# Kernel tuning notes

Hardware: AMD Instinct MI355X
Metric: run time of the kernel (lower is better)

The kernel has to match this reference:

```python
import jax, jax.numpy as jnp
import numpy as np

D_MODEL = 1024
HEAD = 16
K_D = D_MODEL // HEAD
SEQ_LEN = 2048
BATCH = 4
NEG = 1e10


def setup_inputs() -> dict:
    key = jax.random.key(0)
    ks = jax.random.split(key, 5)
    x = jax.random.normal(ks[0], (BATCH, SEQ_LEN, D_MODEL), dtype=jnp.float32)
    # params (torch Linear stored as [out,in]; we store [in,out] and matmul directly)
    W_attn = jax.random.normal(ks[1], (D_MODEL, 3 * D_MODEL), dtype=jnp.float32) * 0.02
    b_attn = jnp.zeros((3 * D_MODEL,), dtype=jnp.float32)
    W_proj = jax.random.normal(ks[2], (D_MODEL, D_MODEL), dtype=jnp.float32) * 0.02
    b_proj = jnp.zeros((D_MODEL,), dtype=jnp.float32)
    return {"x": x, "W_attn": W_attn, "b_attn": b_attn, "W_proj": W_proj, "b_proj": b_proj}


def reference(x, W_attn, b_attn, W_proj, b_proj):
    B, S, D = x.shape
    qkv = x @ W_attn + b_attn                     # [B,S,3D]
    # NOTE: source splits as (value, query, key) in that order
    value, query, key = jnp.split(qkv, 3, axis=-1)

    def heads(t):  # [B,S,D] -> [B,H,S,k_d]
        return t.reshape(B, S, HEAD, K_D).transpose(0, 2, 1, 3)

    v, q, k = heads(value), heads(query), heads(key)
    present = jnp.stack((k, v))                   # [2,B,H,S,k_d]

    scores = jnp.einsum('bhqd,bhkd->bhqk', q, k) / jnp.sqrt(jnp.float32(K_D))
    bias = jnp.tril(jnp.ones((S, S), dtype=scores.dtype))[None, None]
    scores = scores * bias - NEG * (1.0 - bias)
    attn = jax.nn.softmax(scores, axis=-1)
    out = jnp.einsum('bhqk,bhkd->bhqd', attn, v)  # [B,H,S,k_d]
    out = out.transpose(0, 2, 1, 3).reshape(B, S, D)
    out = out @ W_proj + b_proj
    return out, present
```

## Files before the change

kernel.cpp:

```cpp
#include <hip/hip_runtime.h>

typedef __attribute__((ext_vector_type(8))) short short8;
typedef __attribute__((ext_vector_type(4))) short short4v;
typedef __attribute__((ext_vector_type(4))) float f32x4;
typedef __attribute__((ext_vector_type(16))) float f32x16;
typedef __attribute__((ext_vector_type(4))) unsigned int u32x4;
typedef __attribute__((ext_vector_type(2))) unsigned int u32x2;
typedef unsigned int u32;

#define D_MODEL 1024
#define HEADS 16
#define KD 64
#define SEQ 2048
#define BATCH 4
#define NTOK (BATCH*SEQ)
#define QKV_N (3*D_MODEL)

__device__ inline float bf2f(unsigned short u) {
    unsigned x = ((unsigned)u) << 16;
    return __builtin_bit_cast(float, x);
}
__device__ inline unsigned short f2bf(float f) {
    unsigned u = __builtin_bit_cast(unsigned, f);
    u += 0x7FFFu + ((u >> 16) & 1u);
    return (unsigned short)(u >> 16);
}
__device__ __forceinline__ void gload_lds16(const unsigned short* g, unsigned short* l) {
    __builtin_amdgcn_global_load_lds(
        (const __attribute__((address_space(1))) void*)g,
        (__attribute__((address_space(3))) void*)l, 16, 0, 0);
}
__device__ __forceinline__ u32 cvtpk(float lo, float hi) {
    u32 r; asm("v_cvt_pk_bf16_f32 %0, %1, %2" : "=v"(r) : "v"(lo), "v"(hi)); return r;
}
__device__ __forceinline__ void pl32swap(u32& a, u32& b) {
#if __has_builtin(__builtin_amdgcn_permlane32_swap)
    u32x2 r = __builtin_amdgcn_permlane32_swap(a, b, 0, 0);
    a = r[0]; b = r[1];
#else
    u32 pa = (u32)__shfl_xor((int)a, 32, 64);
    u32 pb = (u32)__shfl_xor((int)b, 32, 64);
    bool hb = (threadIdx.x & 32) != 0;
    u32 na = hb ? pb : a;
    u32 nb = hb ? b : pa;
    a = na; b = nb;
#endif
}
__device__ __forceinline__ float pairmax(float x) {
    u32 a = __builtin_bit_cast(u32, x), b = a;
    pl32swap(a, b);
    return fmaxf(x, fmaxf(__builtin_bit_cast(float, a), __builtin_bit_cast(float, b)));
}
__device__ __forceinline__ float pairsum(float x) {
    u32 a = __builtin_bit_cast(u32, x), b = a;
    pl32swap(a, b);
    return __builtin_bit_cast(float, a) + __builtin_bit_cast(float, b);
}

__global__ __launch_bounds__(256) void cvt_kernel(
    const float* __restrict__ x, unsigned short* __restrict__ y)
{
    size_t i = (size_t)blockIdx.x * 256 + threadIdx.x;
    f32x4 a = *reinterpret_cast<const f32x4*>(x + i*8);
    f32x4 b = *reinterpret_cast<const f32x4*>(x + i*8 + 4);
    short8 o;
    #pragma unroll
    for (int j = 0; j < 4; ++j) { o[j] = (short)f2bf(a[j]); o[j+4] = (short)f2bf(b[j]); }
    *reinterpret_cast<short8*>(y + i*8) = o;
}

__global__ __launch_bounds__(256) void transpose_kernel(
    const float* __restrict__ W, unsigned short* __restrict__ WT, int K, int N)
{
    __shared__ unsigned short T[64][80];
    const int tid = threadIdx.x;
    const int n0 = blockIdx.x * 64, k0 = blockIdx.y * 64;

    int r  = tid >> 2;
    int cq = tid & 3;
    const float* src = W + (size_t)(k0 + r) * N + n0 + cq*16;
    #pragma unroll
    for (int q = 0; q < 4; ++q) {
        f32x4 v = *reinterpret_cast<const f32x4*>(src + q*4);
        #pragma unroll
        for (int j = 0; j < 4; ++j) T[cq*16 + q*4 + j][r] = f2bf(v[j]);
    }
    __syncthreads();
    int c  = tid >> 2;
    int rq = tid & 3;
    short8 o0 = *reinterpret_cast<const short8*>(&T[c][rq*16]);
    short8 o1 = *reinterpret_cast<const short8*>(&T[c][rq*16 + 8]);
    unsigned short* dst = WT + (size_t)(n0 + c) * K + k0 + rq*16;
    *reinterpret_cast<short8*>(dst)     = o0;
    *reinterpret_cast<short8*>(dst + 8) = o1;
}

template<int Y_F32, int FUSE>
__global__ __launch_bounds__(256) void gemm_bt_kernel(
    const unsigned short* __restrict__ A, const unsigned short* __restrict__ BT,
    const float* __restrict__ bias, void* __restrict__ Yv,
    unsigned short* __restrict__ vtg, float* __restrict__ pres,
    int M, int N, int K)
{
    __shared__ unsigned short sA[128*64];
    __shared__ unsigned short sB[128*64];

    const int tid = threadIdx.x, lane = tid & 63, w = tid >> 6;
    const int l15 = lane & 15, lg = lane >> 4;

    const int nwg = gridDim.x * gridDim.y;
    const int bid = blockIdx.y * gridDim.x + blockIdx.x;
    const int swz = (bid & 7) * (nwg >> 3) + (bid >> 3);
    const int n0 = (swz % gridDim.x) * 128;
    const int m0 = (swz / gridDim.x) * 128;

    const int wr = w >> 1, wc = w & 1;

    f32x4 acc[4][4];
    #pragma unroll
    for (int m = 0; m < 4; ++m)
        #pragma unroll
        for (int n = 0; n < 4; ++n) acc[m][n] = f32x4{0,0,0,0};

    const int ldrow = (lane >> 3);
    const int slot  = lane & 7;

    for (int k0 = 0; k0 < K; k0 += 64) {
        #pragma unroll
        for (int i = 0; i < 4; ++i) {
            int kb  = w*4 + i;
            int row = kb*8 + ldrow;
            int sc  = slot ^ (row & 7);
            gload_lds16(&A [(size_t)(m0 + row) * K + k0 + sc*8], &sA[kb*512]);
            gload_lds16(&BT[(size_t)(n0 + row) * K + k0 + sc*8], &sB[kb*512]);
        }
        __syncthreads();

        #pragma unroll
        for (int kk = 0; kk < 2; ++kk) {
            short8 af[4], bfr[4];
            #pragma unroll
            for (int m = 0; m < 4; ++m) {
                int row = wr*64 + m*16 + l15;
                int ch  = (4*kk + lg) ^ (row & 7);
                af[m] = *reinterpret_cast<const short8*>(&sA[row*64 + ch*8]);
            }
            #pragma unroll
            for (int n = 0; n < 4; ++n) {
                int row = wc*64 + n*16 + l15;
                int ch  = (4*kk + lg) ^ (row & 7);
                bfr[n] = *reinterpret_cast<const short8*>(&sB[row*64 + ch*8]);
            }
            __builtin_amdgcn_s_setprio(1);
            #pragma unroll
            for (int m = 0; m < 4; ++m)
                #pragma unroll
                for (int n = 0; n < 4; ++n)
                    acc[m][n] = __builtin_amdgcn_mfma_f32_16x16x32_bf16(
                        af[m], bfr[n], acc[m][n], 0, 0, 0);
            __builtin_amdgcn_s_setprio(0);
        }
        __syncthreads();
    }

    #pragma unroll
    for (int n = 0; n < 4; ++n) {
        int col = n0 + wc*64 + n*16 + l15;
        float bv = bias[col];
        #pragma unroll
        for (int m = 0; m < 4; ++m) {
            int row0 = m0 + wr*64 + m*16 + lg*4;
            float v0 = acc[m][n][0] + bv;
            float v1 = acc[m][n][1] + bv;
            float v2 = acc[m][n][2] + bv;
            float v3 = acc[m][n][3] + bv;
            if (Y_F32) {
                float* Y = (float*)Yv;
                Y[(size_t)(row0+0) * N + col] = v0;
                Y[(size_t)(row0+1) * N + col] = v1;
                Y[(size_t)(row0+2) * N + col] = v2;
                Y[(size_t)(row0+3) * N + col] = v3;
            } else {
                unsigned short* Y = (unsigned short*)Yv;
                Y[(size_t)(row0+0) * N + col] = f2bf(v0);
                Y[(size_t)(row0+1) * N + col] = f2bf(v1);
                Y[(size_t)(row0+2) * N + col] = f2bf(v2);
                Y[(size_t)(row0+3) * N + col] = f2bf(v3);
            }
            if (FUSE && n0 < D_MODEL) {
                int hh = col >> 6, dd = col & 63;
                int bb = row0 >> 11, ss = row0 & (SEQ - 1);
                short4v pk;
                pk[0] = (short)f2bf(v0); pk[1] = (short)f2bf(v1);
                pk[2] = (short)f2bf(v2); pk[3] = (short)f2bf(v3);
                *reinterpret_cast<short4v*>(
                    vtg + (((size_t)bb*HEADS + hh)*KD + dd)*SEQ + ss) = pk;
                float* pv = pres + (size_t)BATCH*HEADS*SEQ*KD
                          + (((size_t)bb*HEADS + hh)*SEQ + ss)*KD + dd;
                pv[0] = v0; pv[KD] = v1; pv[2*KD] = v2; pv[3*KD] = v3;
            }
            if (FUSE && n0 >= 2*D_MODEL) {
                int rel = col - 2*D_MODEL;
                int hh = rel >> 6, dd = rel & 63;
                int bb = row0 >> 11, ss = row0 & (SEQ - 1);
                float* pk2 = pres + (((size_t)bb*HEADS + hh)*SEQ + ss)*KD + dd;
                pk2[0] = v0; pk2[KD] = v1; pk2[2*KD] = v2; pk2[3*KD] = v3;
            }
        }
    }
}

__global__ __launch_bounds__(256) void attn_kernel(
    const unsigned short* __restrict__ qkv,
    const unsigned short* __restrict__ vtg,
    unsigned short* __restrict__ aout)
{
    __shared__ unsigned short Kl[2][64*64];
    __shared__ unsigned short Vl[2][64*64];

    const int tid  = threadIdx.x;
    const int lane = tid & 63;
    const int w    = tid >> 6;
    const int l31  = lane & 31, hi = lane >> 5;

    const int bid = blockIdx.x;
    const int hb  = bid & 63;
    const int qb  = 15 - (bid >> 6);
    const int h = hb & 15, b = hb >> 4;

    const unsigned short* base  = qkv + (size_t)b * SEQ * QKV_N;
    const unsigned short* vbase = vtg + ((size_t)b * HEADS + h) * KD * SEQ;
    const int qoff = D_MODEL + h*KD;
    const int koff = 2*D_MODEL + h*KD;

    const float SCALE2 = 0.125f * 1.44269504088896f;
    const float THR_RAW = 44.36f;

    const int ldrow = lane >> 3;
    const int slot  = lane & 7;
    const int ksw   = l31 & 7;

    const int q0 = qb * 128;
    const int qrow  = q0 + w*32 + l31;
    const int qminw = q0 + w*32;

    short8 qf[4];
    #pragma unroll
    for (int ks = 0; ks < 4; ++ks)
        qf[ks] = *reinterpret_cast<const short8*>(
            base + (size_t)qrow * QKV_N + qoff + ks*16 + hi*8);

    f32x16 o0, o1;
    #pragma unroll
    for (int r = 0; r < 16; ++r) { o0[r] = 0.f; o1[r] = 0.f; }
    float m = -1e30f, msc = -1e30f * 0.180336887f, sr = 0.f;

    const int nt = 2*qb + 2;

    #pragma unroll
    for (int i = 0; i < 2; ++i) {
        int kb = w*2 + i, row = kb*8 + ldrow, sc = slot ^ (row & 7);
        gload_lds16(&base[(size_t)row * QKV_N + koff + sc*8], &Kl[0][kb*512]);
        gload_lds16(&vbase[(size_t)row * SEQ + sc*8],         &Vl[0][kb*512]);
    }
    __syncthreads();

    for (int t = 0; t < nt; ++t) {
        const int buf = t & 1;

        if (t + 1 < nt) {
            #pragma unroll
            for (int i = 0; i < 2; ++i) {
                int kb = w*2 + i, row = kb*8 + ldrow, sc = slot ^ (row & 7);
                gload_lds16(&base[(size_t)((t+1)*64 + row) * QKV_N + koff + sc*8],
                            &Kl[buf^1][kb*512]);
                gload_lds16(&vbase[(size_t)row * SEQ + (t+1)*64 + sc*8],
                            &Vl[buf^1][kb*512]);
            }
        }

        const int d0 = qminw - t*64;
        if (d0 > -32) {
            f32x16 sa, sb;
            #pragma unroll
            for (int r = 0; r < 16; ++r) { sa[r] = 0.f; sb[r] = 0.f; }
            __builtin_amdgcn_s_setprio(1);
            #pragma unroll
            for (int ks = 0; ks < 4; ++ks) {
                short8 kf = *reinterpret_cast<const short8*>(
                    &Kl[buf][l31*64 + ((2*ks + hi) ^ ksw)*8]);
                sa = __builtin_amdgcn_mfma_f32_32x32x16_bf16(kf, qf[ks], sa, 0, 0, 0);
            }
            #pragma unroll
            for (int ks = 0; ks < 4; ++ks) {
                short8 kf = *reinterpret_cast<const short8*>(
                    &Kl[buf][(32 + l31)*64 + ((2*ks + hi) ^ ksw)*8]);
                sb = __builtin_amdgcn_mfma_f32_32x32x16_bf16(kf, qf[ks], sb, 0, 0, 0);
            }
            __builtin_amdgcn_s_setprio(0);

            if (d0 <= 32) {
                const int kqA = l31 + d0      - 4*hi;
                const int kqB = l31 + d0 - 32 - 4*hi;
                #pragma unroll
                for (int r = 0; r < 16; ++r) {
                    const int cr = (r & 3) + 8*(r >> 2);
                    if (d0 == 0) sa[r] = (cr <= kqA) ? sa[r] : -1e30f;
                    sb[r] = (cr <= kqB) ? sb[r] : -1e30f;
                }
            }

            float x[8];
            #pragma unroll
            for (int i = 0; i < 8; ++i)
                x[i] = fmaxf(fmaxf(sa[2*i], sa[2*i+1]), fmaxf(sb[2*i], sb[2*i+1]));
            float pm = fmaxf(fmaxf(fmaxf(x[0], x[1]), fmaxf(x[2], x[3])),
                             fmaxf(fmaxf(x[4], x[5]), fmaxf(x[6], x[7])));
            pm = pairmax(pm);
            if (!__all(pm <= m + THR_RAW)) {
                float mn  = fmaxf(m, pm);
                float fac = exp2f((m - mn) * SCALE2);
                sr *= fac;
                #pragma unroll
                for (int r = 0; r < 16; ++r) { o0[r] *= fac; o1[r] *= fac; }
                m = mn; msc = m * SCALE2;
            }

            #pragma unroll
            for (int r = 0; r < 16; ++r) {
                sa[r] = exp2f(sa[r]*SCALE2 - msc);
                sb[r] = exp2f(sb[r]*SCALE2 - msc);
            }
            float u[8];
            #pragma unroll
            for (int i = 0; i < 8; ++i)
                u[i] = (sa[2*i] + sa[2*i+1]) + (sb[2*i] + sb[2*i+1]);
            float ts = ((u[0]+u[1]) + (u[2]+u[3])) + ((u[4]+u[5]) + (u[6]+u[7]));
            sr += pairsum(ts);

            u32 WA[8], WB[8];
            #pragma unroll
            for (int wi = 0; wi < 8; ++wi) {
                WA[wi] = cvtpk(sa[2*wi], sa[2*wi+1]);
                WB[wi] = cvtpk(sb[2*wi], sb[2*wi+1]);
            }

            #pragma unroll
            for (int h32 = 0; h32 < 2; ++h32) {
                #pragma unroll
                for (int ks = 0; ks < 2; ++ks) {
                    u32 W0 = h32 ? WB[4*ks+0] : WA[4*ks+0];
                    u32 W1 = h32 ? WB[4*ks+1] : WA[4*ks+1];
                    u32 W2 = h32 ? WB[4*ks+2] : WA[4*ks+2];
                    u32 W3 = h32 ? WB[4*ks+3] : WA[4*ks+3];
                    u32 s0 = hi ? W0 : W2;
                    u32 s1 = hi ? W1 : W3;
                    u32 r0 = (u32)__shfl_xor((int)s0, 32, 64);
                    u32 r1 = (u32)__shfl_xor((int)s1, 32, 64);
                    u32x4 wv;
                    wv[0] = hi ? r0 : W0;
                    wv[1] = hi ? r1 : W1;
                    wv[2] = hi ? W2 : r0;
                    wv[3] = hi ? W3 : r1;
                    short8 pfrag = __builtin_bit_cast(short8, wv);
                    __builtin_amdgcn_s_setprio(1);
                    #pragma unroll
                    for (int dt = 0; dt < 2; ++dt) {
                        short8 vf = *reinterpret_cast<const short8*>(
                            &Vl[buf][(dt*32 + l31)*64 + ((4*h32 + 2*ks + hi) ^ ksw)*8]);
                        if (dt == 0)
                            o0 = __builtin_amdgcn_mfma_f32_32x32x16_bf16(vf, pfrag, o0, 0, 0, 0);
                        else
                            o1 = __builtin_amdgcn_mfma_f32_32x32x16_bf16(vf, pfrag, o1, 0, 0, 0);
                    }
                    __builtin_amdgcn_s_setprio(0);
                }
            }
        }
        __syncthreads();
    }

    const float inv = 1.0f / sr;
    unsigned short* orow = aout + ((size_t)b * SEQ + qrow) * D_MODEL + h*KD;
    #pragma unroll
    for (int dt = 0; dt < 2; ++dt) {
        #pragma unroll
        for (int g = 0; g < 4; ++g) {
            short4v pk;
            #pragma unroll
            for (int j = 0; j < 4; ++j) {
                float v = (dt == 0 ? o0[4*g + j] : o1[4*g + j]) * inv;
                pk[j] = (short)f2bf(v);
            }
            *reinterpret_cast<short4v*>(orow + dt*32 + 8*g + 4*hi) = pk;
        }
    }
}

extern "C" void kernel_launch(void* const* d_in, const int* in_sizes, int n_in,
                              void* d_out, int out_size, void* d_ws, size_t ws_size,
                              hipStream_t stream)
{
    const float* x      = (const float*)d_in[0];
    const float* W_attn = (const float*)d_in[1];
    const float* b_attn = (const float*)d_in[2];
    const float* W_proj = (const float*)d_in[3];
    const float* b_proj = (const float*)d_in[4];
    float* out = (float*)d_out;

    unsigned short* qkv  = (unsigned short*)d_ws;
    unsigned short* xbf  = qkv + (size_t)NTOK * QKV_N;
    unsigned short* aout = xbf;
    unsigned short* WT   = xbf + (size_t)NTOK * D_MODEL;
    unsigned short* WpT  = WT + (size_t)QKV_N * D_MODEL;
    unsigned short* vtg  = WpT + (size_t)D_MODEL * D_MODEL;
    float* pres = out + (size_t)NTOK * D_MODEL;

    cvt_kernel<<<(NTOK * D_MODEL / 8) / 256, 256, 0, stream>>>(x, xbf);
    dim3 gt1(QKV_N / 64, D_MODEL / 64);
    transpose_kernel<<<gt1, 256, 0, stream>>>(W_attn, WT, D_MODEL, QKV_N);
    dim3 gt2(D_MODEL / 64, D_MODEL / 64);
    transpose_kernel<<<gt2, 256, 0, stream>>>(W_proj, WpT, D_MODEL, D_MODEL);

    dim3 g1(QKV_N / 128, NTOK / 128);
    gemm_bt_kernel<0, 1><<<g1, 256, 0, stream>>>(xbf, WT, b_attn, qkv, vtg, pres,
                                                 NTOK, QKV_N, D_MODEL);

    attn_kernel<<<1024, 256, 0, stream>>>(qkv, vtg, aout);

    dim3 g2(D_MODEL / 128, NTOK / 128);
    gemm_bt_kernel<1, 0><<<g2, 256, 0, stream>>>(aout, WpT, b_proj, out,
                                                 nullptr, nullptr,
                                                 NTOK, D_MODEL, D_MODEL);
}
```

Measured before the change: 215.1 us.

## Double-buffer GEMM LDS tiles with K-step 32 to overlap loads and MFMA

```diff
diff --git a/kernel.cpp b/kernel.cpp
--- a/kernel.cpp
+++ b/kernel.cpp
@@ -102,8 +102,8 @@
     unsigned short* __restrict__ vtg, float* __restrict__ pres,
     int M, int N, int K)
 {
-    __shared__ unsigned short sA[128*64];
-    __shared__ unsigned short sB[128*64];
+    __shared__ unsigned short sA[2][128*32];
+    __shared__ unsigned short sB[2][128*32];
 
     const int tid = threadIdx.x, lane = tid & 63, w = tid >> 6;
     const int l15 = lane & 15, lg = lane >> 4;
@@ -122,44 +122,54 @@
         #pragma unroll
         for (int n = 0; n < 4; ++n) acc[m][n] = f32x4{0,0,0,0};
 
-    const int ldrow = (lane >> 3);
-    const int slot  = lane & 7;
-
-    for (int k0 = 0; k0 < K; k0 += 64) {
-        #pragma unroll
-        for (int i = 0; i < 4; ++i) {
-            int kb  = w*4 + i;
-            int row = kb*8 + ldrow;
-            int sc  = slot ^ (row & 7);
-            gload_lds16(&A [(size_t)(m0 + row) * K + k0 + sc*8], &sA[kb*512]);
-            gload_lds16(&BT[(size_t)(n0 + row) * K + k0 + sc*8], &sB[kb*512]);
-        }
-        __syncthreads();
-
-        #pragma unroll
-        for (int kk = 0; kk < 2; ++kk) {
-            short8 af[4], bfr[4];
-            #pragma unroll
-            for (int m = 0; m < 4; ++m) {
-                int row = wr*64 + m*16 + l15;
-                int ch  = (4*kk + lg) ^ (row & 7);
-                af[m] = *reinterpret_cast<const short8*>(&sA[row*64 + ch*8]);
-            }
-            #pragma unroll
-            for (int n = 0; n < 4; ++n) {
-                int row = wc*64 + n*16 + l15;
-                int ch  = (4*kk + lg) ^ (row & 7);
-                bfr[n] = *reinterpret_cast<const short8*>(&sB[row*64 + ch*8]);
-            }
-            __builtin_amdgcn_s_setprio(1);
-            #pragma unroll
-            for (int m = 0; m < 4; ++m)
-                #pragma unroll
-                for (int n = 0; n < 4; ++n)
-                    acc[m][n] = __builtin_amdgcn_mfma_f32_16x16x32_bf16(
-                        af[m], bfr[n], acc[m][n], 0, 0, 0);
-            __builtin_amdgcn_s_setprio(0);
-        }
+    const int nkt = K >> 5;
+
+    #pragma unroll
+    for (int i = 0; i < 2; ++i) {
+        int slot = i*256 + tid;
+        int row = slot >> 2, c = slot & 3;
+        int sc = c ^ (row & 3);
+        gload_lds16(&A [(size_t)(m0 + row) * K + sc*8], &sA[0][slot*8]);
+        gload_lds16(&BT[(size_t)(n0 + row) * K + sc*8], &sB[0][slot*8]);
+    }
+    __syncthreads();
+
+    for (int kt = 0; kt < nkt; ++kt) {
+        const int buf = kt & 1;
+
+        if (kt + 1 < nkt) {
+            const int k1 = (kt + 1) << 5;
+            #pragma unroll
+            for (int i = 0; i < 2; ++i) {
+                int slot = i*256 + tid;
+                int row = slot >> 2, c = slot & 3;
+                int sc = c ^ (row & 3);
+                gload_lds16(&A [(size_t)(m0 + row) * K + k1 + sc*8], &sA[buf^1][slot*8]);
+                gload_lds16(&BT[(size_t)(n0 + row) * K + k1 + sc*8], &sB[buf^1][slot*8]);
+            }
+        }
+
+        short8 af[4], bfr[4];
+        #pragma unroll
+        for (int m = 0; m < 4; ++m) {
+            int row = wr*64 + m*16 + l15;
+            int ch  = lg ^ (row & 3);
+            af[m] = *reinterpret_cast<const short8*>(&sA[buf][row*32 + ch*8]);
+        }
+        #pragma unroll
+        for (int n = 0; n < 4; ++n) {
+            int row = wc*64 + n*16 + l15;
+            int ch  = lg ^ (row & 3);
+            bfr[n] = *reinterpret_cast<const short8*>(&sB[buf][row*32 + ch*8]);
+        }
+        __builtin_amdgcn_s_setprio(1);
+        #pragma unroll
+        for (int m = 0; m < 4; ++m)
+            #pragma unroll
+            for (int n = 0; n < 4; ++n)
+                acc[m][n] = __builtin_amdgcn_mfma_f32_16x16x32_bf16(
+                    af[m], bfr[n], acc[m][n], 0, 0, 0);
+        __builtin_amdgcn_s_setprio(0);
         __syncthreads();
     }
 
```

New measurement: 225.0 us. +4.6%, slower.
